# Optimization experiments

Measured on AMD Instinct MI355X. Metric: run time of the kernel, lower is better.

Reference implementation:

```python
import jax, jax.numpy as jnp
import numpy as np

SCALE = 1.0  # scale argument passed to titans_memory_forward in the original forward


def setup_inputs() -> dict:
    key = jax.random.key(0)
    k1, k2, k3 = jax.random.split(key, 3)
    B, N, D = 4096, 32768, 1024
    x = jax.random.normal(k1, (B, D), dtype=jnp.float32)
    memory_keys = jax.random.normal(k2, (N, D), dtype=jnp.float32)
    memory_values = jax.random.normal(k3, (N, D), dtype=jnp.float32)
    return {"x": x, "memory_keys": memory_keys, "memory_values": memory_values}


def reference(x, memory_keys, memory_values):
    # Associative memory retrieval: similarity scores -> softmax -> weighted sum of values.
    # scores: [B, N]
    scores = jnp.einsum('bd,nd->bn', x, memory_keys) * SCALE
    attn = jax.nn.softmax(scores, axis=-1)
    # output: [B, D]
    out = jnp.einsum('bn,nd->bd', attn, memory_values)
    return out
```

## Files before the change

kernel.cpp:

```cpp
#include <hip/hip_runtime.h>

typedef _Float16 f16;
typedef _Float16 f16x8 __attribute__((ext_vector_type(8)));
typedef float f32x4 __attribute__((ext_vector_type(4)));

#define B_ 4096
#define N_ 32768
#define D_ 1024
#define BM 32
#define BN 256
#define THREADS 512
#define DSLICE 128
#define NHALF (N_ / 2)
#define ITERS (NHALF / BN)

__device__ __forceinline__ f32x4 mfma16(f16x8 a, f16x8 b, f32x4 c) {
    return __builtin_amdgcn_mfma_f32_16x16x32_f16(a, b, c, 0, 0, 0);
}

__global__ void conv_kf(const float* __restrict__ K, f16* __restrict__ Kf) {
    int tid = blockIdx.x * 256 + threadIdx.x;
    int g = tid >> 6, lane = tid & 63;
    int rb = g >> 5, ks = g & 31;
    int l15 = lane & 15, lg = lane >> 4;
    const float* s = K + (size_t)(rb * 16 + l15) * D_ + ks * 32 + lg * 8;
    float4 a = *(const float4*)s, b = *(const float4*)(s + 4);
    f16x8 h;
    h[0] = (f16)a.x; h[1] = (f16)a.y; h[2] = (f16)a.z; h[3] = (f16)a.w;
    h[4] = (f16)b.x; h[5] = (f16)b.y; h[6] = (f16)b.z; h[7] = (f16)b.w;
    *(f16x8*)(Kf + (size_t)tid * 8) = h;
}

__global__ void conv_vf(const float* __restrict__ V, f16* __restrict__ Vf) {
    int tid = blockIdx.x * 256 + threadIdx.x;
    int g = tid >> 6, lane = tid & 63;
    int db = g & 63, kb = g >> 6;
    int l15 = lane & 15, lg = lane >> 4;
    const float* s = V + (size_t)(kb * 32 + lg * 8) * D_ + db * 16 + l15;
    f16x8 h;
    #pragma unroll
    for (int j = 0; j < 8; ++j) h[j] = (f16)s[(size_t)j * D_];
    *(f16x8*)(Vf + (size_t)tid * 8) = h;
}

__global__ __launch_bounds__(THREADS, 2)
void attn_main(const float* __restrict__ Xg, const f16* __restrict__ Kf,
               const f16* __restrict__ Vf, float* __restrict__ Opart,
               float* __restrict__ Mpart, float* __restrict__ Lpart)
{
    __shared__ __align__(16) f16 Xh[BM * D_];
    __shared__ __align__(16) f16 Pl[2][BM * BN];
    __shared__ float2 red[2][BM][9];

    const int xcd   = blockIdx.x & 7;
    const int chunk = xcd >> 2;
    const int bblk  = ((blockIdx.x >> 3) << 2) | (xcd & 3);
    const int kvbase = chunk * NHALF;
    const int b0 = bblk * BM;
    const int t  = threadIdx.x;

    for (int c = t; c < BM * D_ / 8; c += THREADS) {
        int dblk = c >> 7;
        int row  = (c >> 2) & 31;
        int sub  = c & 3;
        int d0   = dblk * 32 + sub * 8;
        const float* s = Xg + (size_t)(b0 + row) * D_ + d0;
        float4 a = *(const float4*)s, b = *(const float4*)(s + 4);
        f16x8 hi;
        hi[0] = (f16)a.x; hi[1] = (f16)a.y; hi[2] = (f16)a.z; hi[3] = (f16)a.w;
        hi[4] = (f16)b.x; hi[5] = (f16)b.y; hi[6] = (f16)b.z; hi[7] = (f16)b.w;
        *(f16x8*)((char*)Xh + dblk * 2048 + row * 64 + sub * 16) = hi;
    }
    __syncthreads();

    const int wave = t >> 6, lane = t & 63;
    const int l15 = lane & 15, lg = lane >> 4;

    const char* bh0 = (const char*)Xh + l15 * 64 + lg * 16;
    const char* bh1 = (const char*)Xh + (l15 + 16) * 64 + lg * 16;
    const char* pr0 = (const char*)&Pl[0][0] + l15 * 64 + lg * 16;
    const char* pr1 = (const char*)&Pl[0][0] + (l15 + 16) * 64 + lg * 16;

    const f16* kp0 = Kf + ((size_t)(kvbase / 16 + wave * 2) * 32 * 64 + lane) * 8;
    const f16* kp1 = kp0 + 16384;
    const f16* vbase = Vf + (((size_t)(kvbase / 32) * 64 + wave * 8) * 64 + lane) * 8;

    f32x4 S[2][2];
    f16x8 kA[8], kB[8];
    int pbOfs = 0;

    auto LOADK = [&](f16x8* buf, int ks0) {
        #pragma unroll
        for (int j = 0; j < 4; ++j) {
            buf[2 * j]     = *(const f16x8*)(kp0 + (ks0 + j) * 512);
            buf[2 * j + 1] = *(const f16x8*)(kp1 + (ks0 + j) * 512);
        }
    };
    auto USEK = [&](const f16x8* kb2, int ks0) {
        #pragma unroll
        for (int j = 0; j < 4; ++j) {
            int ks = ks0 + j;
            f16x8 ah0 = *(const f16x8*)(bh0 + ks * 2048);
            f16x8 ah1 = *(const f16x8*)(bh1 + ks * 2048);
            __builtin_amdgcn_s_setprio(1);
            S[0][0] = mfma16(ah0, kb2[2 * j],     S[0][0]);
            S[0][1] = mfma16(ah0, kb2[2 * j + 1], S[0][1]);
            S[1][0] = mfma16(ah1, kb2[2 * j],     S[1][0]);
            S[1][1] = mfma16(ah1, kb2[2 * j + 1], S[1][1]);
            __builtin_amdgcn_s_setprio(0);
        }
    };
    auto QK = [&]() {
        #pragma unroll
        for (int rg = 0; rg < 2; ++rg)
            #pragma unroll
            for (int cg = 0; cg < 2; ++cg) S[rg][cg] = (f32x4){0.f, 0.f, 0.f, 0.f};
        LOADK(kA, 0);
        LOADK(kB, 4);  USEK(kA, 0);
        LOADK(kA, 8);  USEK(kB, 4);
        LOADK(kB, 12); USEK(kA, 8);
        LOADK(kA, 16); USEK(kB, 12);
        LOADK(kB, 20); USEK(kA, 16);
        LOADK(kA, 24); USEK(kB, 20);
        LOADK(kB, 28); USEK(kA, 24);
                       USEK(kB, 28);
    };

    f32x4 O[2][8];
    #pragma unroll
    for (int rg = 0; rg < 2; ++rg)
        #pragma unroll
        for (int fn = 0; fn < 8; ++fn) O[rg][fn] = (f32x4){0.f, 0.f, 0.f, 0.f};
    float mq[8];
    #pragma unroll
    for (int u = 0; u < 8; ++u) mq[u] = -INFINITY;
    float m2a = -INFINITY, m2b = -INFINITY, l2a = 0.f, l2b = 0.f;

    f16x8 vA[8], vB[8];
    auto LOADV = [&](f16x8* buf, int ks2) {
        #pragma unroll
        for (int fn = 0; fn < 8; ++fn)
            buf[fn] = *(const f16x8*)(vbase + ks2 * 32768 + fn * 512);
    };
    float ba[8], bb[8];
    auto USEV = [&](const f16x8* vb2, int ks2) {
        f16 ba16 = (f16)ba[ks2], bb16 = (f16)bb[ks2];
        f16x8 pa0 = *(const f16x8*)(pr0 + pbOfs + ks2 * 2048);
        f16x8 pa1 = *(const f16x8*)(pr1 + pbOfs + ks2 * 2048);
        #pragma unroll
        for (int j = 0; j < 8; ++j) { pa0[j] *= ba16; pa1[j] *= bb16; }
        __builtin_amdgcn_s_setprio(1);
        #pragma unroll
        for (int fn = 0; fn < 8; ++fn) {
            O[0][fn] = mfma16(pa0, vb2[fn], O[0][fn]);
            O[1][fn] = mfma16(pa1, vb2[fn], O[1][fn]);
        }
        __builtin_amdgcn_s_setprio(0);
    };

    QK();
    int pb = 0;

    for (int it = 0; it < ITERS; ++it) {
        #pragma unroll
        for (int rg = 0; rg < 2; ++rg)
            #pragma unroll
            for (int i = 0; i < 4; ++i) {
                float a = S[rg][0][i], b = S[rg][1][i];
                float mx = fmaxf(a, b);
                mx = fmaxf(mx, __shfl_xor(mx, 1));
                mx = fmaxf(mx, __shfl_xor(mx, 2));
                mx = fmaxf(mx, __shfl_xor(mx, 4));
                mx = fmaxf(mx, __shfl_xor(mx, 8));
                float p0 = __expf(a - mx), p1 = __expf(b - mx);
                float s = p0 + p1;
                s += __shfl_xor(s, 1);
                s += __shfl_xor(s, 2);
                s += __shfl_xor(s, 4);
                s += __shfl_xor(s, 8);
                int m = rg * 16 + lg * 4 + i;
                int off0 = pb * 16384 + wave * 2048 + m * 64
                         + ((l15 >> 3) << 4) + ((l15 & 7) << 1);
                *(f16*)((char*)&Pl[0][0] + off0)      = (f16)p0;
                *(f16*)((char*)&Pl[0][0] + off0 + 32) = (f16)p1;
                if (l15 == 0) red[pb][m][wave] = make_float2(mx, s);
            }
        __syncthreads();

        pbOfs = pb * 16384;

        LOADV(vA, 0);
        LOADV(vB, 1);

        float m2a0 = m2a, m2b0 = m2b;
        float M2an = m2a, M2bn = m2b;
        #pragma unroll
        for (int s2 = 0; s2 < 8; ++s2) {
            M2an = fmaxf(M2an, red[pb][l15][s2].x);
            M2bn = fmaxf(M2bn, red[pb][l15 + 16][s2].x);
        }
        float laa = 0.f, lbb = 0.f;
        #pragma unroll
        for (int s2 = 0; s2 < 8; ++s2) {
            float2 ra = red[pb][l15][s2], rb = red[pb][l15 + 16][s2];
            ba[s2] = __expf(ra.x - M2an); laa += ra.y * ba[s2];
            bb[s2] = __expf(rb.x - M2bn); lbb += rb.y * bb[s2];
        }
        l2a = l2a * __expf(m2a - M2an) + laa; m2a = M2an;
        l2b = l2b * __expf(m2b - M2bn) + lbb; m2b = M2bn;

        if (__any((M2an > m2a0) || (M2bn > m2b0))) {
            float al[2][4];
            #pragma unroll
            for (int rg = 0; rg < 2; ++rg)
                #pragma unroll
                for (int i = 0; i < 4; ++i) {
                    int u = rg * 4 + i;
                    int src = (lane & 48) | (lg * 4 + i);
                    float Mq = __shfl(rg ? M2bn : M2an, src);
                    al[rg][i] = __expf(mq[u] - Mq);
                    mq[u] = Mq;
                }
            #pragma unroll
            for (int rg = 0; rg < 2; ++rg)
                #pragma unroll
                for (int fn = 0; fn < 8; ++fn)
                    #pragma unroll
                    for (int i = 0; i < 4; ++i)
                        O[rg][fn][i] *= al[rg][i];
        }

        USEV(vA, 0);  LOADV(vA, 2);
        USEV(vB, 1);  LOADV(vB, 3);
        USEV(vA, 2);  LOADV(vA, 4);
        USEV(vB, 3);  LOADV(vB, 5);
        USEV(vA, 4);  LOADV(vA, 6);
        USEV(vB, 5);  LOADV(vB, 7);
        USEV(vA, 6);
        USEV(vB, 7);

        kp0 += (size_t)16 * 16384;
        kp1 += (size_t)16 * 16384;
        vbase += (size_t)8 * 32768;
        if (it + 1 < ITERS) QK();
        pb ^= 1;
    }

    float* Op = Opart + (size_t)chunk * B_ * D_;
    #pragma unroll
    for (int rg = 0; rg < 2; ++rg)
        #pragma unroll
        for (int fn = 0; fn < 8; ++fn)
            #pragma unroll
            for (int i = 0; i < 4; ++i) {
                int row = b0 + rg * 16 + lg * 4 + i;
                int col = wave * DSLICE + fn * 16 + l15;
                Op[(size_t)row * D_ + col] = O[rg][fn][i];
            }
    if (wave == 0 && lg == 0) {
        Mpart[(size_t)chunk * B_ + b0 + l15]      = m2a;
        Lpart[(size_t)chunk * B_ + b0 + l15]      = l2a;
        Mpart[(size_t)chunk * B_ + b0 + 16 + l15] = m2b;
        Lpart[(size_t)chunk * B_ + b0 + 16 + l15] = l2b;
    }
}

__global__ void combine_k(const float* __restrict__ Opart,
                          const float* __restrict__ Mp, const float* __restrict__ Lp,
                          float* __restrict__ Outg)
{
    int b = blockIdx.x;
    float m0 = Mp[b], m1 = Mp[B_ + b];
    float l0 = Lp[b], l1 = Lp[B_ + b];
    float M  = fmaxf(m0, m1);
    float w0 = __expf(m0 - M), w1 = __expf(m1 - M);
    float inv = 1.f / (w0 * l0 + w1 * l1);
    const float4* O0 = (const float4*)(Opart + (size_t)b * D_);
    const float4* O1 = (const float4*)(Opart + (size_t)B_ * D_ + (size_t)b * D_);
    float4* o = (float4*)(Outg + (size_t)b * D_);
    for (int i = threadIdx.x; i < D_ / 4; i += blockDim.x) {
        float4 a = O0[i], c = O1[i];
        float4 r;
        r.x = (w0 * a.x + w1 * c.x) * inv;
        r.y = (w0 * a.y + w1 * c.y) * inv;
        r.z = (w0 * a.z + w1 * c.z) * inv;
        r.w = (w0 * a.w + w1 * c.w) * inv;
        o[i] = r;
    }
}

extern "C" void kernel_launch(void* const* d_in, const int* in_sizes, int n_in,
                              void* d_out, int out_size, void* d_ws, size_t ws_size,
                              hipStream_t stream) {
    const float* X = (const float*)d_in[0];
    const float* K = (const float*)d_in[1];
    const float* V = (const float*)d_in[2];
    float* Out = (float*)d_out;

    const size_t szKf = (size_t)N_ * D_ * sizeof(f16);
    const size_t szVf = (size_t)N_ * D_ * sizeof(f16);
    const size_t szOp = 2ull * B_ * D_ * sizeof(float);
    const size_t szM  = 2ull * B_ * sizeof(float);

    f16*   Kf = (f16*)d_ws;
    f16*   Vf = (f16*)((char*)d_ws + szKf);
    float* Op = (float*)((char*)d_ws + szKf + szVf);
    float* Mp = (float*)((char*)Op + szOp);
    float* Lp = (float*)((char*)Mp + szM);

    conv_kf<<<(N_ * D_ / 8) / 256, 256, 0, stream>>>(K, Kf);
    conv_vf<<<(N_ * D_ / 8) / 256, 256, 0, stream>>>(V, Vf);
    attn_main<<<256, THREADS, 0, stream>>>(X, Kf, Vf, Op, Mp, Lp);
    combine_k<<<B_, 256, 0, stream>>>(Op, Mp, Lp, Out);
}
```

Measured before the change: 876.3 us.

## Double waves per block to 16, halving per-wave key and value slices

Raises the block to 1024 threads (16 waves) with one block per CU. Each wave now computes scores for a single 16-column key strip and accumulates a 64-wide slice of the output. Per-strip softmax rescale factors are recomputed inside the PV step from the shared reduction buffer instead of being kept in registers. The aim is lower register pressure per wave and more waves to hide latency. The cost is a larger cross-wave reduction (16 partials per row), shorter MFMA chains, extra exp calls and more barrier pressure.

```diff
diff --git a/kernel.cpp b/kernel.cpp
--- a/kernel.cpp
+++ b/kernel.cpp
@@ -9,8 +9,8 @@
 #define D_ 1024
 #define BM 32
 #define BN 256
-#define THREADS 512
-#define DSLICE 128
+#define THREADS 1024
+#define DSLICE 64
 #define NHALF (N_ / 2)
 #define ITERS (NHALF / BN)
 
@@ -43,14 +43,14 @@
     *(f16x8*)(Vf + (size_t)tid * 8) = h;
 }
 
-__global__ __launch_bounds__(THREADS, 2)
+__global__ __launch_bounds__(THREADS, 1)
 void attn_main(const float* __restrict__ Xg, const f16* __restrict__ Kf,
                const f16* __restrict__ Vf, float* __restrict__ Opart,
                float* __restrict__ Mpart, float* __restrict__ Lpart)
 {
     __shared__ __align__(16) f16 Xh[BM * D_];
     __shared__ __align__(16) f16 Pl[2][BM * BN];
-    __shared__ float2 red[2][BM][9];
+    __shared__ float2 red[2][BM][17];
 
     const int xcd   = blockIdx.x & 7;
     const int chunk = xcd >> 2;
@@ -81,77 +81,78 @@
     const char* pr0 = (const char*)&Pl[0][0] + l15 * 64 + lg * 16;
     const char* pr1 = (const char*)&Pl[0][0] + (l15 + 16) * 64 + lg * 16;
 
-    const f16* kp0 = Kf + ((size_t)(kvbase / 16 + wave * 2) * 32 * 64 + lane) * 8;
-    const f16* kp1 = kp0 + 16384;
-    const f16* vbase = Vf + (((size_t)(kvbase / 32) * 64 + wave * 8) * 64 + lane) * 8;
-
-    f32x4 S[2][2];
-    f16x8 kA[8], kB[8];
-    int pbOfs = 0;
+    const f16* kp = Kf + ((size_t)(kvbase / 16 + wave) * 2048 + lane) * 8;
+    const f16* vbase = Vf + (((size_t)(kvbase / 32) * 64 + wave * 4) * 64 + lane) * 8;
+
+    f32x4 S0, S1;
+    f16x8 kA[2], kB[2];
+    int pb = 0, pbOfs = 0;
 
     auto LOADK = [&](f16x8* buf, int ks0) {
-        #pragma unroll
-        for (int j = 0; j < 4; ++j) {
-            buf[2 * j]     = *(const f16x8*)(kp0 + (ks0 + j) * 512);
-            buf[2 * j + 1] = *(const f16x8*)(kp1 + (ks0 + j) * 512);
-        }
+        buf[0] = *(const f16x8*)(kp + (ks0    ) * 512);
+        buf[1] = *(const f16x8*)(kp + (ks0 + 1) * 512);
     };
     auto USEK = [&](const f16x8* kb2, int ks0) {
         #pragma unroll
-        for (int j = 0; j < 4; ++j) {
+        for (int j = 0; j < 2; ++j) {
             int ks = ks0 + j;
             f16x8 ah0 = *(const f16x8*)(bh0 + ks * 2048);
             f16x8 ah1 = *(const f16x8*)(bh1 + ks * 2048);
             __builtin_amdgcn_s_setprio(1);
-            S[0][0] = mfma16(ah0, kb2[2 * j],     S[0][0]);
-            S[0][1] = mfma16(ah0, kb2[2 * j + 1], S[0][1]);
-            S[1][0] = mfma16(ah1, kb2[2 * j],     S[1][0]);
-            S[1][1] = mfma16(ah1, kb2[2 * j + 1], S[1][1]);
+            S0 = mfma16(ah0, kb2[j], S0);
+            S1 = mfma16(ah1, kb2[j], S1);
             __builtin_amdgcn_s_setprio(0);
         }
     };
     auto QK = [&]() {
-        #pragma unroll
-        for (int rg = 0; rg < 2; ++rg)
-            #pragma unroll
-            for (int cg = 0; cg < 2; ++cg) S[rg][cg] = (f32x4){0.f, 0.f, 0.f, 0.f};
+        S0 = (f32x4){0.f, 0.f, 0.f, 0.f};
+        S1 = (f32x4){0.f, 0.f, 0.f, 0.f};
         LOADK(kA, 0);
-        LOADK(kB, 4);  USEK(kA, 0);
-        LOADK(kA, 8);  USEK(kB, 4);
-        LOADK(kB, 12); USEK(kA, 8);
-        LOADK(kA, 16); USEK(kB, 12);
-        LOADK(kB, 20); USEK(kA, 16);
-        LOADK(kA, 24); USEK(kB, 20);
-        LOADK(kB, 28); USEK(kA, 24);
-                       USEK(kB, 28);
-    };
-
-    f32x4 O[2][8];
+        LOADK(kB, 2);  USEK(kA, 0);
+        LOADK(kA, 4);  USEK(kB, 2);
+        LOADK(kB, 6);  USEK(kA, 4);
+        LOADK(kA, 8);  USEK(kB, 6);
+        LOADK(kB, 10); USEK(kA, 8);
+        LOADK(kA, 12); USEK(kB, 10);
+        LOADK(kB, 14); USEK(kA, 12);
+        LOADK(kA, 16); USEK(kB, 14);
+        LOADK(kB, 18); USEK(kA, 16);
+        LOADK(kA, 20); USEK(kB, 18);
+        LOADK(kB, 22); USEK(kA, 20);
+        LOADK(kA, 24); USEK(kB, 22);
+        LOADK(kB, 26); USEK(kA, 24);
+        LOADK(kA, 28); USEK(kB, 26);
+        LOADK(kB, 30); USEK(kA, 28);
+                       USEK(kB, 30);
+    };
+
+    f32x4 O[2][4];
     #pragma unroll
     for (int rg = 0; rg < 2; ++rg)
         #pragma unroll
-        for (int fn = 0; fn < 8; ++fn) O[rg][fn] = (f32x4){0.f, 0.f, 0.f, 0.f};
+        for (int fn = 0; fn < 4; ++fn) O[rg][fn] = (f32x4){0.f, 0.f, 0.f, 0.f};
     float mq[8];
     #pragma unroll
     for (int u = 0; u < 8; ++u) mq[u] = -INFINITY;
     float m2a = -INFINITY, m2b = -INFINITY, l2a = 0.f, l2b = 0.f;
 
-    f16x8 vA[8], vB[8];
+    f16x8 vA[4], vB[4];
     auto LOADV = [&](f16x8* buf, int ks2) {
         #pragma unroll
-        for (int fn = 0; fn < 8; ++fn)
+        for (int fn = 0; fn < 4; ++fn)
             buf[fn] = *(const f16x8*)(vbase + ks2 * 32768 + fn * 512);
     };
-    float ba[8], bb[8];
     auto USEV = [&](const f16x8* vb2, int ks2) {
-        f16 ba16 = (f16)ba[ks2], bb16 = (f16)bb[ks2];
+        int strip = ks2 * 2 + (lg >> 1);
+        f16 ba16 = (f16)__expf(red[pb][l15][strip].x - m2a);
+        f16 bb16 = (f16)__expf(red[pb][l15 + 16][strip].x - m2b);
         f16x8 pa0 = *(const f16x8*)(pr0 + pbOfs + ks2 * 2048);
         f16x8 pa1 = *(const f16x8*)(pr1 + pbOfs + ks2 * 2048);
         #pragma unroll
         for (int j = 0; j < 8; ++j) { pa0[j] *= ba16; pa1[j] *= bb16; }
         __builtin_amdgcn_s_setprio(1);
         #pragma unroll
-        for (int fn = 0; fn < 8; ++fn) {
+        for (int fn = 0; fn < 4; ++fn) {
             O[0][fn] = mfma16(pa0, vb2[fn], O[0][fn]);
             O[1][fn] = mfma16(pa1, vb2[fn], O[1][fn]);
         }
@@ -159,30 +160,28 @@
     };
 
     QK();
-    int pb = 0;
 
     for (int it = 0; it < ITERS; ++it) {
         #pragma unroll
         for (int rg = 0; rg < 2; ++rg)
             #pragma unroll
             for (int i = 0; i < 4; ++i) {
-                float a = S[rg][0][i], b = S[rg][1][i];
-                float mx = fmaxf(a, b);
+                float v = rg ? S1[i] : S0[i];
+                float mx = v;
                 mx = fmaxf(mx, __shfl_xor(mx, 1));
                 mx = fmaxf(mx, __shfl_xor(mx, 2));
                 mx = fmaxf(mx, __shfl_xor(mx, 4));
                 mx = fmaxf(mx, __shfl_xor(mx, 8));
-                float p0 = __expf(a - mx), p1 = __expf(b - mx);
-                float s = p0 + p1;
+                float p = __expf(v - mx);
+                float s = p;
                 s += __shfl_xor(s, 1);
                 s += __shfl_xor(s, 2);
                 s += __shfl_xor(s, 4);
                 s += __shfl_xor(s, 8);
                 int m = rg * 16 + lg * 4 + i;
-                int off0 = pb * 16384 + wave * 2048 + m * 64
-                         + ((l15 >> 3) << 4) + ((l15 & 7) << 1);
-                *(f16*)((char*)&Pl[0][0] + off0)      = (f16)p0;
-                *(f16*)((char*)&Pl[0][0] + off0 + 32) = (f16)p1;
+                int off = pb * 16384 + (wave >> 1) * 2048 + m * 64
+                        + ((wave & 1) * 2 + (l15 >> 3)) * 16 + ((l15 & 7) << 1);
+                *(f16*)((char*)&Pl[0][0] + off) = (f16)p;
                 if (l15 == 0) red[pb][m][wave] = make_float2(mx, s);
             }
         __syncthreads();
@@ -195,19 +194,19 @@
         float m2a0 = m2a, m2b0 = m2b;
         float M2an = m2a, M2bn = m2b;
         #pragma unroll
-        for (int s2 = 0; s2 < 8; ++s2) {
+        for (int s2 = 0; s2 < 16; ++s2) {
             M2an = fmaxf(M2an, red[pb][l15][s2].x);
             M2bn = fmaxf(M2bn, red[pb][l15 + 16][s2].x);
         }
         float laa = 0.f, lbb = 0.f;
         #pragma unroll
-        for (int s2 = 0; s2 < 8; ++s2) {
+        for (int s2 = 0; s2 < 16; ++s2) {
             float2 ra = red[pb][l15][s2], rb = red[pb][l15 + 16][s2];
-            ba[s2] = __expf(ra.x - M2an); laa += ra.y * ba[s2];
-            bb[s2] = __expf(rb.x - M2bn); lbb += rb.y * bb[s2];
-        }
-        l2a = l2a * __expf(m2a - M2an) + laa; m2a = M2an;
-        l2b = l2b * __expf(m2b - M2bn) + lbb; m2b = M2bn;
+            laa += __expf(ra.x - M2an) * ra.y;
+            lbb += __expf(rb.x - M2bn) * rb.y;
+        }
+        l2a = l2a * __expf(m2a0 - M2an) + laa; m2a = M2an;
+        l2b = l2b * __expf(m2b0 - M2bn) + lbb; m2b = M2bn;
 
         if (__any((M2an > m2a0) || (M2bn > m2b0))) {
             float al[2][4];
@@ -224,7 +223,7 @@
             #pragma unroll
             for (int rg = 0; rg < 2; ++rg)
                 #pragma unroll
-                for (int fn = 0; fn < 8; ++fn)
+                for (int fn = 0; fn < 4; ++fn)
                     #pragma unroll
                     for (int i = 0; i < 4; ++i)
                         O[rg][fn][i] *= al[rg][i];
@@ -239,8 +238,7 @@
         USEV(vA, 6);
         USEV(vB, 7);
 
-        kp0 += (size_t)16 * 16384;
-        kp1 += (size_t)16 * 16384;
+        kp += (size_t)16 * 16384;
         vbase += (size_t)8 * 32768;
         if (it + 1 < ITERS) QK();
         pb ^= 1;
@@ -250,7 +248,7 @@
     #pragma unroll
     for (int rg = 0; rg < 2; ++rg)
         #pragma unroll
-        for (int fn = 0; fn < 8; ++fn)
+        for (int fn = 0; fn < 4; ++fn)
             #pragma unroll
             for (int i = 0; i < 4; ++i) {
                 int row = b0 + rg * 16 + lg * 4 + i;
```

New measurement: 2.220 ms. 2.53x slower.

## Prefetch next tile's first K fragments during PV phase and relax launch bounds

Applied to the files above, without the earlier changes.

Issues the first two K fragment loads for the next iteration before the PV accumulation instead of after it, so their global latency overlaps the V MFMAs. The QK phase of the next tile then starts with registers already populated. Launch bounds drop from 2 to 1 block per SM to give the extra live registers (kA/kB alongside vA/vB and O) room without spilling. The cost is lower occupancy, which reduces latency hiding across blocks.

```diff
diff --git a/kernel.cpp b/kernel.cpp
--- a/kernel.cpp
+++ b/kernel.cpp
@@ -43,7 +43,7 @@
     *(f16x8*)(Vf + (size_t)tid * 8) = h;
 }
 
-__global__ __launch_bounds__(THREADS, 2)
+__global__ __launch_bounds__(THREADS, 1)
 void attn_main(const float* __restrict__ Xg, const f16* __restrict__ Kf,
                const f16* __restrict__ Vf, float* __restrict__ Opart,
                float* __restrict__ Mpart, float* __restrict__ Lpart)
@@ -83,6 +83,7 @@
 
     const f16* kp0 = Kf + ((size_t)(kvbase / 16 + wave * 2) * 32 * 64 + lane) * 8;
     const f16* kp1 = kp0 + 16384;
+    const size_t KADV = (size_t)16 * 16384;
     const f16* vbase = Vf + (((size_t)(kvbase / 32) * 64 + wave * 8) * 64 + lane) * 8;
 
     f32x4 S[2][2];
@@ -94,6 +95,13 @@
         for (int j = 0; j < 4; ++j) {
             buf[2 * j]     = *(const f16x8*)(kp0 + (ks0 + j) * 512);
             buf[2 * j + 1] = *(const f16x8*)(kp1 + (ks0 + j) * 512);
+        }
+    };
+    auto LOADKN = [&](f16x8* buf, int ks0) {
+        #pragma unroll
+        for (int j = 0; j < 4; ++j) {
+            buf[2 * j]     = *(const f16x8*)(kp0 + KADV + (ks0 + j) * 512);
+            buf[2 * j + 1] = *(const f16x8*)(kp1 + KADV + (ks0 + j) * 512);
         }
     };
     auto USEK = [&](const f16x8* kb2, int ks0) {
@@ -110,11 +118,14 @@
             __builtin_amdgcn_s_setprio(0);
         }
     };
+    auto ZEROS = [&]() {
+        #pragma unroll
+        for (int rg = 0; rg < 2; ++rg)
+            #pragma unroll
+            for (int cg = 0; cg < 2; ++cg) S[rg][cg] = (f32x4){0.f, 0.f, 0.f, 0.f};
+    };
     auto QK = [&]() {
-        #pragma unroll
-        for (int rg = 0; rg < 2; ++rg)
-            #pragma unroll
-            for (int cg = 0; cg < 2; ++cg) S[rg][cg] = (f32x4){0.f, 0.f, 0.f, 0.f};
+        ZEROS();
         LOADK(kA, 0);
         LOADK(kB, 4);  USEK(kA, 0);
         LOADK(kA, 8);  USEK(kB, 4);
@@ -162,6 +173,8 @@
     int pb = 0;
 
     for (int it = 0; it < ITERS; ++it) {
+        const bool more = (it + 1 < ITERS);
+
         #pragma unroll
         for (int rg = 0; rg < 2; ++rg)
             #pragma unroll
@@ -189,6 +202,10 @@
 
         pbOfs = pb * 16384;
 
+        if (more) {
+            LOADKN(kA, 0);
+            LOADKN(kB, 4);
+        }
         LOADV(vA, 0);
         LOADV(vB, 1);
 
@@ -239,10 +256,20 @@
         USEV(vA, 6);
         USEV(vB, 7);
 
-        kp0 += (size_t)16 * 16384;
-        kp1 += (size_t)16 * 16384;
+        kp0 += KADV;
+        kp1 += KADV;
         vbase += (size_t)8 * 32768;
-        if (it + 1 < ITERS) QK();
+        if (more) {
+            ZEROS();
+            USEK(kA, 0);  LOADK(kA, 8);
+            USEK(kB, 4);  LOADK(kB, 12);
+            USEK(kA, 8);  LOADK(kA, 16);
+            USEK(kB, 12); LOADK(kB, 20);
+            USEK(kA, 16); LOADK(kA, 24);
+            USEK(kB, 20); LOADK(kB, 28);
+            USEK(kA, 24);
+            USEK(kB, 28);
+        }
         pb ^= 1;
     }
 
```

Measured after the change: 1.361 ms. +55.3%, slower.
